# Kernel tuning notes

Hardware: AMD Instinct MI355X
Metric: run time of the kernel (lower is better)

Reference implementation:

```python
import jax, jax.numpy as jnp
import numpy as np

EMBED_DIM = 1024
HEAD_DIM = 128
SEQ = 2048
BATCH = 16


def setup_inputs() -> dict:
    key = jax.random.key(0)
    ks = jax.random.split(key, 7)
    s = 1.0 / np.sqrt(EMBED_DIM)
    return {
        "x": jax.random.normal(ks[0], (BATCH, SEQ, EMBED_DIM), dtype=jnp.float32),
        "Wq": jax.random.uniform(ks[1], (EMBED_DIM, HEAD_DIM), jnp.float32, -s, s),
        "bq": jax.random.uniform(ks[2], (HEAD_DIM,), jnp.float32, -s, s),
        "Wk": jax.random.uniform(ks[3], (EMBED_DIM, HEAD_DIM), jnp.float32, -s, s),
        "bk": jax.random.uniform(ks[4], (HEAD_DIM,), jnp.float32, -s, s),
        "Wv": jax.random.uniform(ks[5], (EMBED_DIM, HEAD_DIM), jnp.float32, -s, s),
        "bv": jax.random.uniform(ks[6], (HEAD_DIM,), jnp.float32, -s, s),
    }


def reference(x, Wq, bq, Wk, bk, Wv, bv):
    # q,k,v: [B,S,Dh]
    q = x @ Wq + bq
    k = x @ Wk + bk
    v = x @ Wv + bv
    # NOTE: original module MULTIPLIES by embed_dim**0.5 (faithful to source).
    scale = jnp.asarray(EMBED_DIM ** 0.5, dtype=x.dtype)
    scores = jnp.einsum("bqd,bkd->bqk", q, k) * scale  # [B,S,S]
    causal = jnp.tril(jnp.ones((SEQ, SEQ), dtype=bool))
    scores = jnp.where(causal, scores, -jnp.inf)
    attn = jax.nn.softmax(scores, axis=-1)
    # dropout_rate=0 -> identity
    return jnp.einsum("bqk,bkd->bqd", attn, v)
```

## Files before the change

kernel.cpp:

```cpp
#include <hip/hip_runtime.h>

#define BATCH 16
#define SEQ   2048
#define EMB   1024
#define DH    128

typedef _Float16 half4_t __attribute__((ext_vector_type(4)));
typedef _Float16 half8_t __attribute__((ext_vector_type(8)));
typedef float    f32x4   __attribute__((ext_vector_type(4)));

#define OFF_WT2 0u
#define OFF_QHI 0x200000u
#define OFF_QLO (OFF_QHI + 0x800000u)
#define OFF_KHI (OFF_QLO + 0x800000u)
#define OFF_KLO (OFF_KHI + 0x800000u)
#define OFF_VT  (OFF_KLO + 0x800000u)

__device__ __forceinline__ void gload16(const void* g, void* l) {
    __builtin_amdgcn_global_load_lds(
        (__attribute__((address_space(1))) const unsigned int*)g,
        (__attribute__((address_space(3))) unsigned int*)l, 16, 0, 0);
}

__global__ __launch_bounds__(256) void prep_w(
    const float* __restrict__ Wq, const float* __restrict__ Wk,
    const float* __restrict__ Wv, _Float16* __restrict__ Wt2) {
    const int t  = blockIdx.x * 256 + threadIdx.x;
    const int kc = t / 2560, rem = t % 2560;
    const int lo = rem >= 1536 ? 1 : 0;
    const int rr = lo ? rem - 1536 : rem;
    const int nt = rr >> 6, c = rr & 63;
    const int g = c >> 4, r = c & 15;
    const int k0 = kc * 32 + g * 8;
    const float* W; int col;
    if (nt < 8)       { W = Wq; col = nt * 16 + r; }
    else if (nt < 16) { W = Wk; col = (nt - 8) * 16 + r; }
    else              { W = Wv; col = (nt - 16) * 16 + r; }
    half8_t v;
#pragma unroll
    for (int j = 0; j < 8; ++j) {
        float f = W[(size_t)(k0 + j) * DH + col];
        _Float16 h = (_Float16)f;
        v[j] = lo ? (_Float16)(f - (float)h) : h;
    }
    *(half8_t*)((char*)Wt2 + (size_t)kc * 40960 + (lo ? 24576 : 0)
                + (size_t)nt * 1024 + c * 16) = v;
}

#define XBUF  0
#define FHI   32768
#define FLO   40960

__global__ __launch_bounds__(256, 2) void proj_qkv(
    const float* __restrict__ x, const _Float16* __restrict__ Wt2,
    const float* __restrict__ bq, const float* __restrict__ bk,
    const float* __restrict__ bv,
    char* __restrict__ qhi, char* __restrict__ qlo,
    char* __restrict__ khi, char* __restrict__ klo,
    char* __restrict__ vt) {
    __shared__ __align__(16) char lds[49152];
    const int tid = threadIdx.x, lane = tid & 63, w = tid >> 6;
    const int l15 = lane & 15, g = lane >> 4;
    const int m0  = blockIdx.x * 64;

    f32x4 acc[4][6];
#pragma unroll
    for (int mt = 0; mt < 4; ++mt)
#pragma unroll
        for (int j = 0; j < 6; ++j) acc[mt][j] = {};

    auto stage_x = [&](int t, int buf) {
#pragma unroll
        for (int i = 0; i < 4; ++i) {
            const int cb = w * 256 + i * 64;
            const int sidx = cb + lane;
            const int r = sidx >> 4, s = sidx & 15;
            const int c = s ^ (r & 7);
            gload16(x + (size_t)(m0 + r) * EMB + t * 64 + c * 4,
                    lds + XBUF + buf * 16384 + cb * 16);
        }
    };

    auto loadW = [&](int kc, half8_t (&wh)[6], half8_t (&wl)[4]) {
        const char* p = (const char*)Wt2 + (size_t)kc * 40960 + lane * 16;
#pragma unroll
        for (int j = 0; j < 6; ++j) {
            const int nt = (j >> 1) * 8 + (j & 1) * 4 + w;
            wh[j] = *(const half8_t*)(p + nt * 1024);
        }
#pragma unroll
        for (int j = 0; j < 4; ++j) {
            const int nt = (j >> 1) * 8 + (j & 1) * 4 + w;
            wl[j] = *(const half8_t*)(p + 24576 + nt * 1024);
        }
    };

    auto compute = [&](int s, const half8_t (&Wh)[6], const half8_t (&Wl)[4]) {
#pragma unroll
        for (int mt = 0; mt < 4; ++mt) {
            const int RR = mt * 16 + l15;
            const int sl = ((s * 4 + g) ^ (l15 & 7)) * 16;
            half8_t xh = *(const half8_t*)(lds + FHI + RR * 128 + sl);
            half8_t xl = *(const half8_t*)(lds + FLO + RR * 128 + sl);
#pragma unroll
            for (int j = 0; j < 6; ++j) {
                acc[mt][j] = __builtin_amdgcn_mfma_f32_16x16x32_f16(xh, Wh[j], acc[mt][j], 0, 0, 0);
                if (j < 4) {
                    acc[mt][j] = __builtin_amdgcn_mfma_f32_16x16x32_f16(xl, Wh[j], acc[mt][j], 0, 0, 0);
                    acc[mt][j] = __builtin_amdgcn_mfma_f32_16x16x32_f16(xh, Wl[j], acc[mt][j], 0, 0, 0);
                }
            }
        }
    };

    stage_x(0, 0);

    for (int t = 0; t < 16; ++t) {
        __syncthreads();

        half8_t Wh0[6], Wl0[4], Wh1[6], Wl1[4];
        loadW(2 * t,     Wh0, Wl0);
        loadW(2 * t + 1, Wh1, Wl1);
        __builtin_amdgcn_sched_barrier(0);

#pragma unroll
        for (int u = 0; u < 2; ++u) {
            const char* Xb = lds + XBUF + (t & 1) * 16384;
            const int R = (tid >> 3) + u * 32;
            const int o = tid & 7;
            const int rx = R & 7;
            f32x4 a0 = *(const f32x4*)(Xb + R * 256 + ((o * 2)     ^ rx) * 16);
            f32x4 a1 = *(const f32x4*)(Xb + R * 256 + ((o * 2 + 1) ^ rx) * 16);
            half8_t hi, lo;
#pragma unroll
            for (int jj = 0; jj < 4; ++jj) {
                float f = a0[jj]; _Float16 h = (_Float16)f;
                hi[jj] = h; lo[jj] = (_Float16)(f - (float)h);
                float f2 = a1[jj]; _Float16 h2 = (_Float16)f2;
                hi[jj + 4] = h2; lo[jj + 4] = (_Float16)(f2 - (float)h2);
            }
            *(half8_t*)(lds + FHI + R * 128 + (o ^ rx) * 16) = hi;
            *(half8_t*)(lds + FLO + R * 128 + (o ^ rx) * 16) = lo;
        }

#pragma unroll
        for (int j = 0; j < 6; ++j) { asm volatile("" :: "v"(Wh0[j]), "v"(Wh1[j])); }
#pragma unroll
        for (int j = 0; j < 4; ++j) { asm volatile("" :: "v"(Wl0[j]), "v"(Wl1[j])); }

        __syncthreads();

        if (t < 15) stage_x(t + 1, (t + 1) & 1);
        __builtin_amdgcn_sched_barrier(0);

        compute(0, Wh0, Wl0);
        compute(1, Wh1, Wl1);
    }

    __syncthreads();
    float* scr = (float*)(lds + FHI + w * 1280);
    const float SC = 46.166241308446828f;

#pragma unroll
    for (int j = 0; j < 6; ++j) {
        const int nt = (j >> 1) * 8 + (j & 1) * 4 + w;
        float bias;
        if (j < 2)      bias = bq[nt * 16 + l15];
        else if (j < 4) bias = bk[(nt - 8) * 16 + l15];
        else            bias = bv[(nt - 16) * 16 + l15];
#pragma unroll
        for (int mt = 0; mt < 4; ++mt) {
            f32x4 a = acc[mt][j];
#pragma unroll
            for (int r = 0; r < 4; ++r) {
                float v = a[r] + bias;
                if (j < 2) v *= SC;
                scr[(g * 4 + r) * 20 + l15] = v;
            }
            if (j < 4) {
                f32x4 tv = *(const f32x4*)(scr + l15 * 20 + g * 4);
                half4_t h4, l4;
#pragma unroll
                for (int r = 0; r < 4; ++r) {
                    _Float16 h = (_Float16)tv[r];
                    h4[r] = h; l4[r] = (_Float16)(tv[r] - (float)h);
                }
                const int tIdx = m0 / 16 + mt;
                const int oct  = 2 * nt + (g >> 1);
                const int octm = (j < 2) ? oct : oct - 16;
                const size_t off = (size_t)tIdx * 4096 + (octm >> 2) * 1024
                                 + (octm & 3) * 256 + l15 * 16 + (g & 1) * 8;
                char* dh_ = (j < 2) ? qhi : khi;
                char* dl_ = (j < 2) ? qlo : klo;
                *(half4_t*)(dh_ + off) = h4;
                *(half4_t*)(dl_ + off) = l4;
            } else {
                half4_t v4;
#pragma unroll
                for (int r = 0; r < 4; ++r)
                    v4[r] = (_Float16)scr[(g * 4 + r) * 20 + l15];
                const int s0 = (m0 & (SEQ - 1)) + mt * 16;
                const int b  = m0 >> 11;
                const size_t off = ((size_t)b * 64 + (s0 >> 5)) * 8192
                                 + ((s0 >> 4) & 1) * 4096 + (nt - 16) * 512
                                 + g * 128 + l15 * 8;
                *(half4_t*)(vt + off) = v4;
            }
        }
    }
}

__global__ __launch_bounds__(512) void attn(
    const char* __restrict__ qhi, const char* __restrict__ qlo,
    const char* __restrict__ khi, const char* __restrict__ klo,
    const char* __restrict__ vt, float* __restrict__ out) {
    __shared__ __align__(16) char lds[49152];
    const int tid = threadIdx.x, lane = tid & 63, w = tid >> 6;
    const int l15 = lane & 15, g = lane >> 4;
    const int gid = blockIdx.x;
    const int b   = ((gid & 7) << 1) | ((gid >> 3) & 1);
    const int pr  = gid >> 4;
    const int jt  = (w < 4) ? (31 - pr) : pr;
    const int wq  = w & 3;
    const int qw0 = jt * 64 + wq * 16;
    const int nkv = 2 * (32 - pr);

    auto stage = [&](int t, int buf) {
        char* dst = lds + buf * 24576;
        const size_t kb4 = ((size_t)b * 128 + t * 2) * 4096;
        const size_t vb8 = ((size_t)b * 64 + t) * 8192;
        const int off = w * 1024;
        gload16(khi + kb4 + off + lane * 16, dst + off);
        gload16(klo + kb4 + off + lane * 16, dst + 8192 + off);
        gload16(vt  + vb8 + off + lane * 16, dst + 16384 + off);
    };

    const size_t qt4 = ((size_t)b * 128 + (qw0 >> 4)) * 4096;
    half8_t Qh[4], Ql[4];
#pragma unroll
    for (int kk = 0; kk < 4; ++kk) {
        const size_t o = qt4 + kk * 1024 + g * 256 + l15 * 16;
        Qh[kk] = *(const half8_t*)(qhi + o);
        Ql[kk] = *(const half8_t*)(qlo + o);
    }

    f32x4 o[8];
#pragma unroll
    for (int dt = 0; dt < 8; ++dt) o[dt] = {};
    float mrun = -3.0e38f, ell = 0.0f;

    stage(0, 0);

    for (int t = 0; t < nkv; ++t) {
        __syncthreads();
        if (t + 1 < nkv) stage(t + 1, (t + 1) & 1);

        const int kb = t * 32;
        if (kb <= qw0 + 15) {
            const char* kbuf = lds + (t & 1) * 24576;

            f32x4 sa0 = {}, sb0 = {}, sa1 = {}, sb1 = {};
#pragma unroll
            for (int kk = 0; kk < 4; ++kk) {
                const int fo = kk * 1024 + g * 256 + l15 * 16;
                half8_t kh0 = *(const half8_t*)(kbuf + fo);
                half8_t kl0 = *(const half8_t*)(kbuf + 8192 + fo);
                half8_t kh1 = *(const half8_t*)(kbuf + 4096 + fo);
                half8_t kl1 = *(const half8_t*)(kbuf + 12288 + fo);
                sa0 = __builtin_amdgcn_mfma_f32_16x16x32_f16(kh0, Qh[kk], sa0, 0, 0, 0);
                sb0 = __builtin_amdgcn_mfma_f32_16x16x32_f16(kl0, Qh[kk], sb0, 0, 0, 0);
                sb0 = __builtin_amdgcn_mfma_f32_16x16x32_f16(kh0, Ql[kk], sb0, 0, 0, 0);
                sa1 = __builtin_amdgcn_mfma_f32_16x16x32_f16(kh1, Qh[kk], sa1, 0, 0, 0);
                sb1 = __builtin_amdgcn_mfma_f32_16x16x32_f16(kl1, Qh[kk], sb1, 0, 0, 0);
                sb1 = __builtin_amdgcn_mfma_f32_16x16x32_f16(kh1, Ql[kk], sb1, 0, 0, 0);
            }
            f32x4 s0 = sa0 + sb0, s1 = sa1 + sb1;

            if (kb + 31 > qw0) {
#pragma unroll
                for (int r = 0; r < 4; ++r) {
                    if (kb + g * 4 + r      > qw0 + l15) s0[r] = -3.0e38f;
                    if (kb + 16 + g * 4 + r > qw0 + l15) s1[r] = -3.0e38f;
                }
            }

            float mt = fmaxf(fmaxf(fmaxf(s0[0], s0[1]), fmaxf(s0[2], s0[3])),
                             fmaxf(fmaxf(s1[0], s1[1]), fmaxf(s1[2], s1[3])));
            mt = fmaxf(mt, __shfl_xor(mt, 16, 64));
            mt = fmaxf(mt, __shfl_xor(mt, 32, 64));
            if (!__all(mt <= mrun + 8.0f)) {
                const float mnew = fmaxf(mrun, mt);
                const float alpha = exp2f(mrun - mnew);
                ell *= alpha;
#pragma unroll
                for (int dt = 0; dt < 8; ++dt) o[dt] *= alpha;
                mrun = mnew;
            }
            float p[8];
#pragma unroll
            for (int r = 0; r < 4; ++r) {
                p[r]     = exp2f(s0[r] - mrun);
                p[4 + r] = exp2f(s1[r] - mrun);
            }
            float ps = ((p[0] + p[1]) + (p[2] + p[3])) + ((p[4] + p[5]) + (p[6] + p[7]));
            ps += __shfl_xor(ps, 16, 64);
            ps += __shfl_xor(ps, 32, 64);
            ell += ps;

            half4_t pf0, pf1;
#pragma unroll
            for (int r = 0; r < 4; ++r) { pf0[r] = (_Float16)p[r]; pf1[r] = (_Float16)p[4 + r]; }

            const char* vbuf = kbuf + 16384;
#pragma unroll
            for (int dt = 0; dt < 8; ++dt) {
                const int vo = dt * 512 + g * 128 + l15 * 8;
                half4_t v0 = *(const half4_t*)(vbuf + vo);
                half4_t v1 = *(const half4_t*)(vbuf + 4096 + vo);
                o[dt] = __builtin_amdgcn_mfma_f32_16x16x16f16(v0, pf0, o[dt], 0, 0, 0);
                o[dt] = __builtin_amdgcn_mfma_f32_16x16x16f16(v1, pf1, o[dt], 0, 0, 0);
            }
        }
    }

    const float rinv = 1.0f / ell;
    float* orow = out + ((size_t)b * SEQ + qw0 + l15) * DH + g * 4;
#pragma unroll
    for (int dt = 0; dt < 8; ++dt) {
        f32x4 ov = o[dt] * rinv;
        *(f32x4*)(orow + dt * 16) = ov;
    }
}

extern "C" void kernel_launch(void* const* d_in, const int* in_sizes, int n_in,
                              void* d_out, int out_size, void* d_ws, size_t ws_size,
                              hipStream_t stream) {
    const float* x  = (const float*)d_in[0];
    const float* Wq = (const float*)d_in[1];
    const float* bq = (const float*)d_in[2];
    const float* Wk = (const float*)d_in[3];
    const float* bk = (const float*)d_in[4];
    const float* Wv = (const float*)d_in[5];
    const float* bv = (const float*)d_in[6];
    float* out = (float*)d_out;

    char* ws = (char*)d_ws;
    _Float16* Wt2 = (_Float16*)(ws + OFF_WT2);
    char* q_hi = ws + OFF_QHI;
    char* q_lo = ws + OFF_QLO;
    char* k_hi = ws + OFF_KHI;
    char* k_lo = ws + OFF_KLO;
    char* v_t  = ws + OFF_VT;

    prep_w  <<<320, 256, 0, stream>>>(Wq, Wk, Wv, Wt2);
    proj_qkv<<<512, 256, 0, stream>>>(x, Wt2, bq, bk, bv, q_hi, q_lo, k_hi, k_lo, v_t);
    attn    <<<256, 512, 0, stream>>>(q_hi, q_lo, k_hi, k_lo, v_t, out);
}
```

Before: 142.3 us.

## Retile QKV projection to 128-row blocks with 8 waves; add MFMA priority hints

The projection kernel now uses 512-thread blocks covering 128 rows, with each of 8 waves owning one 16-column slice of Q, K and V instead of 4 waves owning several. This halves the number of weight fragments each wave loads per k-chunk and doubles reuse of each staged x tile, in exchange for doubled LDS use (96KB) and possibly lower occupancy. The attention kernel also wraps its MFMA loops in s_setprio raises so matrix instructions get issue priority over other waves.

```diff
diff --git a/kernel.cpp b/kernel.cpp
--- a/kernel.cpp
+++ b/kernel.cpp
@@ -48,26 +48,26 @@
 }
 
 #define XBUF  0
-#define FHI   32768
-#define FLO   40960
-
-__global__ __launch_bounds__(256, 2) void proj_qkv(
+#define FHI   65536
+#define FLO   81920
+
+__global__ __launch_bounds__(512, 2) void proj_qkv(
     const float* __restrict__ x, const _Float16* __restrict__ Wt2,
     const float* __restrict__ bq, const float* __restrict__ bk,
     const float* __restrict__ bv,
     char* __restrict__ qhi, char* __restrict__ qlo,
     char* __restrict__ khi, char* __restrict__ klo,
     char* __restrict__ vt) {
-    __shared__ __align__(16) char lds[49152];
+    __shared__ __align__(16) char lds[98304];
     const int tid = threadIdx.x, lane = tid & 63, w = tid >> 6;
     const int l15 = lane & 15, g = lane >> 4;
-    const int m0  = blockIdx.x * 64;
-
-    f32x4 acc[4][6];
-#pragma unroll
-    for (int mt = 0; mt < 4; ++mt)
-#pragma unroll
-        for (int j = 0; j < 6; ++j) acc[mt][j] = {};
+    const int m0  = blockIdx.x * 128;
+
+    f32x4 acc[8][3];
+#pragma unroll
+    for (int mt = 0; mt < 8; ++mt)
+#pragma unroll
+        for (int j = 0; j < 3; ++j) acc[mt][j] = {};
 
     auto stage_x = [&](int t, int buf) {
 #pragma unroll
@@ -77,39 +77,35 @@
             const int r = sidx >> 4, s = sidx & 15;
             const int c = s ^ (r & 7);
             gload16(x + (size_t)(m0 + r) * EMB + t * 64 + c * 4,
-                    lds + XBUF + buf * 16384 + cb * 16);
+                    lds + XBUF + buf * 32768 + cb * 16);
         }
     };
 
-    auto loadW = [&](int kc, half8_t (&wh)[6], half8_t (&wl)[4]) {
+    auto loadW = [&](int kc, half8_t& qh, half8_t& ql, half8_t& kh,
+                     half8_t& kl, half8_t& vh) {
         const char* p = (const char*)Wt2 + (size_t)kc * 40960 + lane * 16;
-#pragma unroll
-        for (int j = 0; j < 6; ++j) {
-            const int nt = (j >> 1) * 8 + (j & 1) * 4 + w;
-            wh[j] = *(const half8_t*)(p + nt * 1024);
-        }
-#pragma unroll
-        for (int j = 0; j < 4; ++j) {
-            const int nt = (j >> 1) * 8 + (j & 1) * 4 + w;
-            wl[j] = *(const half8_t*)(p + 24576 + nt * 1024);
-        }
+        qh = *(const half8_t*)(p + (size_t)w * 1024);
+        ql = *(const half8_t*)(p + 24576 + (size_t)w * 1024);
+        kh = *(const half8_t*)(p + (size_t)(8 + w) * 1024);
+        kl = *(const half8_t*)(p + 24576 + (size_t)(8 + w) * 1024);
+        vh = *(const half8_t*)(p + (size_t)(16 + w) * 1024);
     };
 
-    auto compute = [&](int s, const half8_t (&Wh)[6], const half8_t (&Wl)[4]) {
-#pragma unroll
-        for (int mt = 0; mt < 4; ++mt) {
+    auto compute = [&](int s, const half8_t& qh, const half8_t& ql,
+                       const half8_t& kh, const half8_t& kl, const half8_t& vh) {
+#pragma unroll
+        for (int mt = 0; mt < 8; ++mt) {
             const int RR = mt * 16 + l15;
             const int sl = ((s * 4 + g) ^ (l15 & 7)) * 16;
             half8_t xh = *(const half8_t*)(lds + FHI + RR * 128 + sl);
             half8_t xl = *(const half8_t*)(lds + FLO + RR * 128 + sl);
-#pragma unroll
-            for (int j = 0; j < 6; ++j) {
-                acc[mt][j] = __builtin_amdgcn_mfma_f32_16x16x32_f16(xh, Wh[j], acc[mt][j], 0, 0, 0);
-                if (j < 4) {
-                    acc[mt][j] = __builtin_amdgcn_mfma_f32_16x16x32_f16(xl, Wh[j], acc[mt][j], 0, 0, 0);
-                    acc[mt][j] = __builtin_amdgcn_mfma_f32_16x16x32_f16(xh, Wl[j], acc[mt][j], 0, 0, 0);
-                }
-            }
+            acc[mt][0] = __builtin_amdgcn_mfma_f32_16x16x32_f16(xh, qh, acc[mt][0], 0, 0, 0);
+            acc[mt][0] = __builtin_amdgcn_mfma_f32_16x16x32_f16(xl, qh, acc[mt][0], 0, 0, 0);
+            acc[mt][0] = __builtin_amdgcn_mfma_f32_16x16x32_f16(xh, ql, acc[mt][0], 0, 0, 0);
+            acc[mt][1] = __builtin_amdgcn_mfma_f32_16x16x32_f16(xh, kh, acc[mt][1], 0, 0, 0);
+            acc[mt][1] = __builtin_amdgcn_mfma_f32_16x16x32_f16(xl, kh, acc[mt][1], 0, 0, 0);
+            acc[mt][1] = __builtin_amdgcn_mfma_f32_16x16x32_f16(xh, kl, acc[mt][1], 0, 0, 0);
+            acc[mt][2] = __builtin_amdgcn_mfma_f32_16x16x32_f16(xh, vh, acc[mt][2], 0, 0, 0);
         }
     };
 
@@ -118,16 +114,17 @@
     for (int t = 0; t < 16; ++t) {
         __syncthreads();
 
-        half8_t Wh0[6], Wl0[4], Wh1[6], Wl1[4];
-        loadW(2 * t,     Wh0, Wl0);
-        loadW(2 * t + 1, Wh1, Wl1);
+        half8_t qh0, ql0, kh0, kl0, vh0, qh1, ql1, kh1, kl1, vh1;
+        loadW(2 * t,     qh0, ql0, kh0, kl0, vh0);
+        loadW(2 * t + 1, qh1, ql1, kh1, kl1, vh1);
         __builtin_amdgcn_sched_barrier(0);
 
 #pragma unroll
         for (int u = 0; u < 2; ++u) {
-            const char* Xb = lds + XBUF + (t & 1) * 16384;
-            const int R = (tid >> 3) + u * 32;
-            const int o = tid & 7;
+            const char* Xb = lds + XBUF + (t & 1) * 32768;
+            const int task = tid + u * 512;
+            const int R = task >> 3;
+            const int o = task & 7;
             const int rx = R & 7;
             f32x4 a0 = *(const f32x4*)(Xb + R * 256 + ((o * 2)     ^ rx) * 16);
             f32x4 a1 = *(const f32x4*)(Xb + R * 256 + ((o * 2 + 1) ^ rx) * 16);
@@ -143,41 +140,38 @@
             *(half8_t*)(lds + FLO + R * 128 + (o ^ rx) * 16) = lo;
         }
 
-#pragma unroll
-        for (int j = 0; j < 6; ++j) { asm volatile("" :: "v"(Wh0[j]), "v"(Wh1[j])); }
-#pragma unroll
-        for (int j = 0; j < 4; ++j) { asm volatile("" :: "v"(Wl0[j]), "v"(Wl1[j])); }
+        asm volatile("" :: "v"(qh0), "v"(ql0), "v"(kh0), "v"(kl0), "v"(vh0));
+        asm volatile("" :: "v"(qh1), "v"(ql1), "v"(kh1), "v"(kl1), "v"(vh1));
 
         __syncthreads();
 
         if (t < 15) stage_x(t + 1, (t + 1) & 1);
         __builtin_amdgcn_sched_barrier(0);
 
-        compute(0, Wh0, Wl0);
-        compute(1, Wh1, Wl1);
+        compute(0, qh0, ql0, kh0, kl0, vh0);
+        compute(1, qh1, ql1, kh1, kl1, vh1);
     }
 
     __syncthreads();
-    float* scr = (float*)(lds + FHI + w * 1280);
+    float* scr = (float*)(lds + (size_t)w * 1280);
     const float SC = 46.166241308446828f;
 
 #pragma unroll
-    for (int j = 0; j < 6; ++j) {
-        const int nt = (j >> 1) * 8 + (j & 1) * 4 + w;
+    for (int j = 0; j < 3; ++j) {
         float bias;
-        if (j < 2)      bias = bq[nt * 16 + l15];
-        else if (j < 4) bias = bk[(nt - 8) * 16 + l15];
-        else            bias = bv[(nt - 16) * 16 + l15];
-#pragma unroll
-        for (int mt = 0; mt < 4; ++mt) {
+        if (j == 0)      bias = bq[w * 16 + l15];
+        else if (j == 1) bias = bk[w * 16 + l15];
+        else             bias = bv[w * 16 + l15];
+#pragma unroll
+        for (int mt = 0; mt < 8; ++mt) {
             f32x4 a = acc[mt][j];
 #pragma unroll
             for (int r = 0; r < 4; ++r) {
                 float v = a[r] + bias;
-                if (j < 2) v *= SC;
+                if (j == 0) v *= SC;
                 scr[(g * 4 + r) * 20 + l15] = v;
             }
-            if (j < 4) {
+            if (j < 2) {
                 f32x4 tv = *(const f32x4*)(scr + l15 * 20 + g * 4);
                 half4_t h4, l4;
 #pragma unroll
@@ -185,13 +179,12 @@
                     _Float16 h = (_Float16)tv[r];
                     h4[r] = h; l4[r] = (_Float16)(tv[r] - (float)h);
                 }
-                const int tIdx = m0 / 16 + mt;
-                const int oct  = 2 * nt + (g >> 1);
-                const int octm = (j < 2) ? oct : oct - 16;
+                const int tIdx = blockIdx.x * 8 + mt;
+                const int octm = 2 * w + (g >> 1);
                 const size_t off = (size_t)tIdx * 4096 + (octm >> 2) * 1024
                                  + (octm & 3) * 256 + l15 * 16 + (g & 1) * 8;
-                char* dh_ = (j < 2) ? qhi : khi;
-                char* dl_ = (j < 2) ? qlo : klo;
+                char* dh_ = (j == 0) ? qhi : khi;
+                char* dl_ = (j == 0) ? qlo : klo;
                 *(half4_t*)(dh_ + off) = h4;
                 *(half4_t*)(dl_ + off) = l4;
             } else {
@@ -202,7 +195,7 @@
                 const int s0 = (m0 & (SEQ - 1)) + mt * 16;
                 const int b  = m0 >> 11;
                 const size_t off = ((size_t)b * 64 + (s0 >> 5)) * 8192
-                                 + ((s0 >> 4) & 1) * 4096 + (nt - 16) * 512
+                                 + ((s0 >> 4) & 1) * 4096 + (size_t)w * 512
                                  + g * 128 + l15 * 8;
                 *(half4_t*)(vt + off) = v4;
             }
@@ -260,6 +253,7 @@
             const char* kbuf = lds + (t & 1) * 24576;
 
             f32x4 sa0 = {}, sb0 = {}, sa1 = {}, sb1 = {};
+            __builtin_amdgcn_s_setprio(1);
 #pragma unroll
             for (int kk = 0; kk < 4; ++kk) {
                 const int fo = kk * 1024 + g * 256 + l15 * 16;
@@ -274,6 +268,7 @@
                 sb1 = __builtin_amdgcn_mfma_f32_16x16x32_f16(kl1, Qh[kk], sb1, 0, 0, 0);
                 sb1 = __builtin_amdgcn_mfma_f32_16x16x32_f16(kh1, Ql[kk], sb1, 0, 0, 0);
             }
+            __builtin_amdgcn_s_setprio(0);
             f32x4 s0 = sa0 + sb0, s1 = sa1 + sb1;
 
             if (kb + 31 > qw0) {
@@ -312,6 +307,7 @@
             for (int r = 0; r < 4; ++r) { pf0[r] = (_Float16)p[r]; pf1[r] = (_Float16)p[4 + r]; }
 
             const char* vbuf = kbuf + 16384;
+            __builtin_amdgcn_s_setprio(1);
 #pragma unroll
             for (int dt = 0; dt < 8; ++dt) {
                 const int vo = dt * 512 + g * 128 + l15 * 8;
@@ -320,6 +316,7 @@
                 o[dt] = __builtin_amdgcn_mfma_f32_16x16x16f16(v0, pf0, o[dt], 0, 0, 0);
                 o[dt] = __builtin_amdgcn_mfma_f32_16x16x16f16(v1, pf1, o[dt], 0, 0, 0);
             }
+            __builtin_amdgcn_s_setprio(0);
         }
     }
 
@@ -353,6 +350,6 @@
     char* v_t  = ws + OFF_VT;
 
     prep_w  <<<320, 256, 0, stream>>>(Wq, Wk, Wv, Wt2);
-    proj_qkv<<<512, 256, 0, stream>>>(x, Wt2, bq, bk, bv, q_hi, q_lo, k_hi, k_lo, v_t);
+    proj_qkv<<<256, 512, 0, stream>>>(x, Wt2, bq, bk, bv, q_hi, q_lo, k_hi, k_lo, v_t);
     attn    <<<256, 512, 0, stream>>>(q_hi, q_lo, k_hi, k_lo, v_t, out);
 }
```

Measured after the change: 140.9 us. No clear change (-1.0%).
